# Optimization experiments

Measured on AMD Instinct MI355X. Metric: run time of the kernel, lower is better.

## Reference

```python
import jax, jax.numpy as jnp
import numpy as np

D_MODEL, D_K, D_V = 512, 64, 64
B, S = 8, 4096


def setup_inputs() -> dict:
    key = jax.random.key(0)
    ks = jax.random.split(key, 10)
    scale = 1.0 / np.sqrt(D_MODEL)
    return {
        "q": jax.random.normal(ks[0], (B, S, D_MODEL), dtype=jnp.float32),
        "k": jax.random.normal(ks[1], (B, S, D_MODEL), dtype=jnp.float32),
        "v": jax.random.normal(ks[2], (B, S, D_MODEL), dtype=jnp.float32),
        "mask": jax.random.randint(ks[3], (B, S), 0, 2, dtype=jnp.int32),
        "Wq": jax.random.uniform(ks[4], (D_MODEL, D_K), jnp.float32, -scale, scale),
        "bq": jax.random.uniform(ks[5], (D_K,), jnp.float32, -scale, scale),
        "Wk": jax.random.uniform(ks[6], (D_MODEL, D_K), jnp.float32, -scale, scale),
        "bk": jax.random.uniform(ks[7], (D_K,), jnp.float32, -scale, scale),
        "Wv": jax.random.uniform(ks[8], (D_MODEL, D_V), jnp.float32, -scale, scale),
        "bv": jax.random.uniform(ks[9], (D_V,), jnp.float32, -scale, scale),
    }


def reference(q, k, v, mask, Wq, bq, Wk, bk, Wv, bv):
    # single-head QKV projections
    qh = jnp.einsum("bsd,dk->bsk", q, Wq) + bq  # [B,S,d_k]
    kh = jnp.einsum("bsd,dk->bsk", k, Wk) + bk  # [B,S,d_k]
    vh = jnp.einsum("bsd,dv->bsv", v, Wv) + bv  # [B,S,d_v]
    scores = jnp.einsum("bqk,bsk->bqs", qh, kh) / jnp.sqrt(jnp.float32(D_K))
    # key-padding mask: mask [B,S] -> [B,1,S], masked positions -> -1e10
    scores = jnp.where(mask[:, None, :] == 0, jnp.float32(-1e10), scores)
    attn = jax.nn.softmax(scores, axis=-1)
    return jnp.einsum("bqs,bsv->bqv", attn, vh)
```

## Files before the change

kernel.cpp:

```cpp
#include <hip/hip_runtime.h>

typedef __attribute__((ext_vector_type(8))) short bf16x8;
typedef __attribute__((ext_vector_type(4))) float f32x4;
typedef __attribute__((ext_vector_type(4))) unsigned short u16x4;

__device__ __forceinline__ short f2bf(float f) {
  unsigned int u = __builtin_bit_cast(unsigned int, f);
  u += 0x7fffu + ((u >> 16) & 1u);
  return (short)(u >> 16);
}

__global__ void prep_w(const float* __restrict__ Wq, const float* __restrict__ Wk,
                       const float* __restrict__ Wv, unsigned short* __restrict__ wt) {
  int idx = blockIdx.x * 256 + threadIdx.x;
  int m = idx >> 15;
  int rem = idx & 32767;
  int n = rem >> 9;
  int k = rem & 511;
  const float* W = (m == 0) ? Wq : ((m == 1) ? Wk : Wv);
  wt[idx] = (unsigned short)f2bf(W[k * 64 + n]);
}

__global__ __launch_bounds__(256) void proj_kernel(
    const float* __restrict__ qx, const float* __restrict__ kx, const float* __restrict__ vx,
    const unsigned short* __restrict__ wt, const int* __restrict__ mask,
    const float* __restrict__ bqp, const float* __restrict__ bkp, const float* __restrict__ bvp,
    unsigned short* __restrict__ qo, unsigned short* __restrict__ ko,
    unsigned short* __restrict__ vo) {
  __shared__ unsigned short lds[64 * 256];
  const int mode = blockIdx.y;
  const float* x = (mode == 0) ? qx : ((mode == 1) ? kx : vx);
  const float* bias = (mode == 0) ? bqp : ((mode == 1) ? bkp : bvp);
  const unsigned short* wtm = wt + mode * (64 * 512);
  const float osc = (mode == 0) ? 0.18033688011112042f : 1.0f;

  const int tid = threadIdx.x;
  const int w = tid >> 6, lane = tid & 63;
  const int g = lane >> 4, ln = lane & 15;
  const int rowbase = blockIdx.x * 128;

  const f32x4 fz = {0.f, 0.f, 0.f, 0.f};
  f32x4 acc[2][4];
#pragma unroll
  for (int mi = 0; mi < 2; ++mi)
#pragma unroll
    for (int nf = 0; nf < 4; ++nf) acc[mi][nf] = fz;

  for (int half = 0; half < 2; ++half) {
    __syncthreads();
#pragma unroll
    for (int i = 0; i < 8; ++i) {
      int c = tid + i * 256;
      int n = c >> 5, kc = c & 31;
      bf16x8 d = *reinterpret_cast<const bf16x8*>(wtm + n * 512 + half * 256 + kc * 8);
      int bo = (n * 512 + kc * 16) ^ ((n & 7) << 4);
      *reinterpret_cast<bf16x8*>(reinterpret_cast<char*>(lds) + bo) = d;
    }
    __syncthreads();
#pragma unroll
    for (int ks = 0; ks < 8; ++ks) {
      bf16x8 afrag[2];
#pragma unroll
      for (int mi = 0; mi < 2; ++mi) {
        int row = rowbase + w * 32 + mi * 16 + ln;
        const float4* ap = reinterpret_cast<const float4*>(
            x + (size_t)row * 512 + half * 256 + ks * 32 + g * 8);
        float4 a0 = ap[0], a1 = ap[1];
        bf16x8 af;
        af[0] = f2bf(a0.x); af[1] = f2bf(a0.y); af[2] = f2bf(a0.z); af[3] = f2bf(a0.w);
        af[4] = f2bf(a1.x); af[5] = f2bf(a1.y); af[6] = f2bf(a1.z); af[7] = f2bf(a1.w);
        afrag[mi] = af;
      }
#pragma unroll
      for (int nf = 0; nf < 4; ++nf) {
        int n = nf * 16 + ln;
        int bo = (n * 512 + ks * 64 + g * 16) ^ ((n & 7) << 4);
        bf16x8 bfrag = *reinterpret_cast<const bf16x8*>(reinterpret_cast<const char*>(lds) + bo);
        acc[0][nf] = __builtin_amdgcn_mfma_f32_16x16x32_bf16(afrag[0], bfrag, acc[0][nf], 0, 0, 0);
        acc[1][nf] = __builtin_amdgcn_mfma_f32_16x16x32_bf16(afrag[1], bfrag, acc[1][nf], 0, 0, 0);
      }
    }
  }

  float bc[4];
#pragma unroll
  for (int nf = 0; nf < 4; ++nf) bc[nf] = bias[nf * 16 + ln];

  if (mode < 2) {
    unsigned short* o = (mode == 0) ? qo : ko;
#pragma unroll
    for (int mi = 0; mi < 2; ++mi)
#pragma unroll
      for (int nf = 0; nf < 4; ++nf)
#pragma unroll
        for (int r = 0; r < 4; ++r) {
          int row = rowbase + w * 32 + mi * 16 + g * 4 + r;
          o[(size_t)row * 64 + nf * 16 + ln] = (unsigned short)f2bf((acc[mi][nf][r] + bc[nf]) * osc);
        }
  } else {
    __syncthreads();
#pragma unroll
    for (int mi = 0; mi < 2; ++mi)
#pragma unroll
      for (int nf = 0; nf < 4; ++nf)
#pragma unroll
        for (int r = 0; r < 4; ++r) {
          int srow = w * 32 + mi * 16 + g * 4 + r;
          lds[srow * 64 + nf * 16 + ln] = (unsigned short)f2bf(acc[mi][nf][r] + bc[nf]);
        }
    __syncthreads();
    int b = rowbase >> 12, s0 = rowbase & 4095;
    int dv = tid & 63, sc = tid >> 6;
#pragma unroll
    for (int i = 0; i < 4; ++i) {
      int sbase = s0 + sc * 32 + i * 8;
      const int* mrow = mask + b * 4096 + sbase;
      bf16x8 pack;
#pragma unroll
      for (int j = 0; j < 8; ++j) {
        short vv = (short)lds[(sc * 32 + i * 8 + j) * 64 + dv];
        pack[j] = mrow[j] ? vv : (short)0;
      }
      *reinterpret_cast<bf16x8*>(vo + (size_t)(b * 64 + dv) * 4096 + sbase) = pack;
    }
  }
}

#define KVBLK 128
#define NT 16

__global__ __launch_bounds__(256, 2) void attn_kernel(
    const unsigned short* __restrict__ qh, const unsigned short* __restrict__ kh,
    const unsigned short* __restrict__ vt, const int* __restrict__ mask,
    float* __restrict__ out0, float* __restrict__ out1,
    float* __restrict__ l0p, float* __restrict__ l1p) {
  __shared__ unsigned short kt[2][KVBLK * 64];
  __shared__ unsigned short vv[2][80 * 128];

  const int b = blockIdx.y;
  const int z = blockIdx.z;
  const int kv0 = z * (NT * KVBLK);
  float* __restrict__ optr = z ? out1 : out0;
  float* __restrict__ lptr = z ? l1p : l0p;
  const int qbase = blockIdx.x * 128;
  const int tid = threadIdx.x;
  const int w = tid >> 6, lane = tid & 63;
  const int g = lane >> 4, ln = lane & 15;

  for (int i = tid; i < 15 * 128; i += 256) {
    vv[0][65 * 128 + i] = 0;
    vv[1][65 * 128 + i] = 0;
  }

  bf16x8 qa[2][2];
#pragma unroll
  for (int qf = 0; qf < 2; ++qf) {
    int row = qbase + w * 32 + qf * 16 + ln;
    const unsigned short* qp = qh + (size_t)(b * 4096 + row) * 64;
    qa[qf][0] = *reinterpret_cast<const bf16x8*>(qp + g * 8);
    qa[qf][1] = *reinterpret_cast<const bf16x8*>(qp + 32 + g * 8);
  }

  const f32x4 fz = {0.f, 0.f, 0.f, 0.f};
  f32x4 accO[2][5];
#pragma unroll
  for (int qf = 0; qf < 2; ++qf)
#pragma unroll
    for (int nf = 0; nf < 5; ++nf) accO[qf][nf] = fz;

  const unsigned short* khb = kh + (size_t)b * 4096 * 64;
  const unsigned short* vtb = vt + (size_t)b * 64 * 4096;

  bf16x8 kreg[4], vreg[4];
  int mreg = 0;
  auto issue = [&](int ti) {
    int kvbase = kv0 + ti * KVBLK;
#pragma unroll
    for (int i = 0; i < 4; ++i) {
      int c = tid + i * 256;
      vreg[i] = *reinterpret_cast<const bf16x8*>(vtb + (size_t)(c >> 4) * 4096 + kvbase + (c & 15) * 8);
      kreg[i] = *reinterpret_cast<const bf16x8*>(khb + (size_t)(kvbase + (c >> 3)) * 64 + (c & 7) * 8);
    }
    if (tid < KVBLK) mreg = mask[b * 4096 + kvbase + tid];
  };
  auto commit = [&](int bs) {
#pragma unroll
    for (int i = 0; i < 4; ++i) {
      int c = tid + i * 256;
      int kbo = ((c >> 3) * 128 + (c & 7) * 16) ^ (((c >> 3) & 7) << 4);
      *reinterpret_cast<bf16x8*>(reinterpret_cast<char*>(kt[bs]) + kbo) = kreg[i];
      int dv = c >> 4;
      int P0 = (c & 15) * 8;
      int c2 = P0 >> 5, h = (P0 >> 4) & 1, gg = (P0 >> 2) & 3;
      int x1 = 32 * c2 + 8 * gg + 4 * h;
      int swz = (dv & 7) << 4;
      union { bf16x8 v; u16x4 h4[2]; } sp; sp.v = vreg[i];
      *reinterpret_cast<u16x4*>(reinterpret_cast<char*>(vv[bs]) + ((dv * 256 + 2 * x1) ^ swz)) = sp.h4[0];
      *reinterpret_cast<u16x4*>(reinterpret_cast<char*>(vv[bs]) + ((dv * 256 + 2 * x1 + 16) ^ swz)) = sp.h4[1];
    }
    if (tid < KVBLK) {
      int p = tid;
      int x = 32 * (p >> 5) + 8 * ((p >> 2) & 3) + 4 * ((p >> 4) & 1) + (p & 3);
      vv[bs][64 * 128 + x] = mreg ? (unsigned short)0x3F80 : (unsigned short)0;
    }
  };

  issue(0);
  commit(0);
  __syncthreads();
  int cur = 0;

  for (int ti = 0; ti < NT; ++ti) {
    if (ti + 1 < NT) issue(ti + 1);

    f32x4 s0[8], s1[8];
#pragma unroll
    for (int nf = 0; nf < 8; ++nf) { s0[nf] = fz; s1[nf] = fz; }
    __builtin_amdgcn_s_setprio(1);
#pragma unroll
    for (int c2 = 0; c2 < 2; ++c2)
#pragma unroll
      for (int nf = 0; nf < 8; ++nf) {
        int kvr = nf * 16 + ln;
        int bo = (kvr * 128 + c2 * 64 + g * 16) ^ ((kvr & 7) << 4);
        bf16x8 kf = *reinterpret_cast<const bf16x8*>(reinterpret_cast<const char*>(kt[cur]) + bo);
        s0[nf] = __builtin_amdgcn_mfma_f32_16x16x32_bf16(kf, qa[0][c2], s0[nf], 0, 0, 0);
        s1[nf] = __builtin_amdgcn_mfma_f32_16x16x32_bf16(kf, qa[1][c2], s1[nf], 0, 0, 0);
      }
    __builtin_amdgcn_s_setprio(0);

    unsigned int pw[2][4][4];
#pragma unroll
    for (int c2 = 0; c2 < 4; ++c2)
#pragma unroll
      for (int hh = 0; hh < 2; ++hh) {
        {
          float p0 = __builtin_exp2f(s0[2 * c2 + hh][0]);
          float p1 = __builtin_exp2f(s0[2 * c2 + hh][1]);
          float p2 = __builtin_exp2f(s0[2 * c2 + hh][2]);
          float p3 = __builtin_exp2f(s0[2 * c2 + hh][3]);
          unsigned int w0, w1;
          asm("v_cvt_pk_bf16_f32 %0, %1, %2" : "=v"(w0) : "v"(p0), "v"(p1));
          asm("v_cvt_pk_bf16_f32 %0, %1, %2" : "=v"(w1) : "v"(p2), "v"(p3));
          pw[0][c2][2 * hh] = w0;
          pw[0][c2][2 * hh + 1] = w1;
        }
        {
          float p0 = __builtin_exp2f(s1[2 * c2 + hh][0]);
          float p1 = __builtin_exp2f(s1[2 * c2 + hh][1]);
          float p2 = __builtin_exp2f(s1[2 * c2 + hh][2]);
          float p3 = __builtin_exp2f(s1[2 * c2 + hh][3]);
          unsigned int w0, w1;
          asm("v_cvt_pk_bf16_f32 %0, %1, %2" : "=v"(w0) : "v"(p0), "v"(p1));
          asm("v_cvt_pk_bf16_f32 %0, %1, %2" : "=v"(w1) : "v"(p2), "v"(p3));
          pw[1][c2][2 * hh] = w0;
          pw[1][c2][2 * hh + 1] = w1;
        }
      }

    __builtin_amdgcn_s_setprio(1);
#pragma unroll
    for (int c2 = 0; c2 < 4; ++c2) {
      union { unsigned int u[4]; bf16x8 v; } pa0, pa1;
#pragma unroll
      for (int t = 0; t < 4; ++t) { pa0.u[t] = pw[0][c2][t]; pa1.u[t] = pw[1][c2][t]; }
#pragma unroll
      for (int nf = 0; nf < 5; ++nf) {
        int dvr = nf * 16 + ln;
        int bo = (dvr * 256 + c2 * 64 + g * 16) ^ ((dvr & 7) << 4);
        bf16x8 vb = *reinterpret_cast<const bf16x8*>(reinterpret_cast<const char*>(vv[cur]) + bo);
        accO[0][nf] = __builtin_amdgcn_mfma_f32_16x16x32_bf16(pa0.v, vb, accO[0][nf], 0, 0, 0);
        accO[1][nf] = __builtin_amdgcn_mfma_f32_16x16x32_bf16(pa1.v, vb, accO[1][nf], 0, 0, 0);
      }
    }
    __builtin_amdgcn_s_setprio(0);

    if (ti + 1 < NT) commit(cur ^ 1);
    __syncthreads();
    cur ^= 1;
  }

#pragma unroll
  for (int qf = 0; qf < 2; ++qf)
#pragma unroll
    for (int r = 0; r < 4; ++r) {
      int grow = b * 4096 + qbase + w * 32 + qf * 16 + g * 4 + r;
#pragma unroll
      for (int nf = 0; nf < 4; ++nf)
        optr[(size_t)grow * 64 + nf * 16 + ln] = accO[qf][nf][r];
      if (ln == 0) lptr[grow] = accO[qf][4][r];
    }
}

__global__ __launch_bounds__(256) void combine_kernel(
    float* __restrict__ out, const float* __restrict__ po1,
    const float* __restrict__ l0p, const float* __restrict__ l1p) {
  int idx = blockIdx.x * 256 + threadIdx.x;
  int row = idx >> 4;
  float rl = 1.0f / (l0p[row] + l1p[row]);
  float4 a = reinterpret_cast<float4*>(out)[idx];
  float4 c = reinterpret_cast<const float4*>(po1)[idx];
  a.x = (a.x + c.x) * rl;
  a.y = (a.y + c.y) * rl;
  a.z = (a.z + c.z) * rl;
  a.w = (a.w + c.w) * rl;
  reinterpret_cast<float4*>(out)[idx] = a;
}

extern "C" void kernel_launch(void* const* d_in, const int* in_sizes, int n_in,
                              void* d_out, int out_size, void* d_ws, size_t ws_size,
                              hipStream_t stream) {
  const float* q = (const float*)d_in[0];
  const float* k = (const float*)d_in[1];
  const float* v = (const float*)d_in[2];
  const int* mask = (const int*)d_in[3];
  const float* Wq = (const float*)d_in[4];
  const float* bq = (const float*)d_in[5];
  const float* Wk = (const float*)d_in[6];
  const float* bk = (const float*)d_in[7];
  const float* Wv = (const float*)d_in[8];
  const float* bv = (const float*)d_in[9];

  char* wsb = (char*)d_ws;
  unsigned short* qh = (unsigned short*)(wsb);
  unsigned short* kh = (unsigned short*)(wsb + (4u << 20));
  unsigned short* vt = (unsigned short*)(wsb + (8u << 20));
  unsigned short* wt = (unsigned short*)(wsb + (12u << 20));
  float* po1 = (float*)(wsb + (12u << 20) + 196608);
  float* l0p = (float*)(wsb + (12u << 20) + 196608 + (8u << 20));
  float* l1p = l0p + 32768;

  prep_w<<<384, 256, 0, stream>>>(Wq, Wk, Wv, wt);
  proj_kernel<<<dim3(256, 3), 256, 0, stream>>>(q, k, v, wt, mask, bq, bk, bv, qh, kh, vt);
  attn_kernel<<<dim3(32, 8, 2), 256, 0, stream>>>(qh, kh, vt, mask,
                                                  (float*)d_out, po1, l0p, l1p);
  combine_kernel<<<2048, 256, 0, stream>>>((float*)d_out, po1, l0p, l1p);
}
```

Baseline: 111.8 us.

## Halve projection tile rows, prefetch activations, and raise occupancy

The projection kernel now handles 64 rows per block instead of 128, launching twice as many blocks, and sets launch bounds to target 5 blocks per CU. The activation loads are software-pipelined: each iteration issues the next k-slice's float4 loads before converting and multiplying the current one. The second weight half is staged mid-loop. This is meant to hide global-memory latency on the memory-bound fp32 activation stream, at the cost of staging the weights twice as often across blocks.

New measurement: 111.2 us. About the same (-0.6%).

```diff
diff --git a/kernel.cpp b/kernel.cpp
--- a/kernel.cpp
+++ b/kernel.cpp
@@ -21,7 +21,7 @@
   wt[idx] = (unsigned short)f2bf(W[k * 64 + n]);
 }
 
-__global__ __launch_bounds__(256) void proj_kernel(
+__global__ __launch_bounds__(256, 5) void proj_kernel(
     const float* __restrict__ qx, const float* __restrict__ kx, const float* __restrict__ vx,
     const unsigned short* __restrict__ wt, const int* __restrict__ mask,
     const float* __restrict__ bqp, const float* __restrict__ bkp, const float* __restrict__ bvp,
@@ -37,17 +37,16 @@
   const int tid = threadIdx.x;
   const int w = tid >> 6, lane = tid & 63;
   const int g = lane >> 4, ln = lane & 15;
-  const int rowbase = blockIdx.x * 128;
+  const int rowbase = blockIdx.x * 64;
 
   const f32x4 fz = {0.f, 0.f, 0.f, 0.f};
-  f32x4 acc[2][4];
-#pragma unroll
-  for (int mi = 0; mi < 2; ++mi)
-#pragma unroll
-    for (int nf = 0; nf < 4; ++nf) acc[mi][nf] = fz;
-
-  for (int half = 0; half < 2; ++half) {
-    __syncthreads();
+  f32x4 acc[4];
+#pragma unroll
+  for (int nf = 0; nf < 4; ++nf) acc[nf] = fz;
+
+  const float* xrow = x + (size_t)(rowbase + w * 16 + ln) * 512 + g * 8;
+
+  auto stageW = [&](int half) {
 #pragma unroll
     for (int i = 0; i < 8; ++i) {
       int c = tid + i * 256;
@@ -56,30 +55,39 @@
       int bo = (n * 512 + kc * 16) ^ ((n & 7) << 4);
       *reinterpret_cast<bf16x8*>(reinterpret_cast<char*>(lds) + bo) = d;
     }
-    __syncthreads();
-#pragma unroll
-    for (int ks = 0; ks < 8; ++ks) {
-      bf16x8 afrag[2];
-#pragma unroll
-      for (int mi = 0; mi < 2; ++mi) {
-        int row = rowbase + w * 32 + mi * 16 + ln;
-        const float4* ap = reinterpret_cast<const float4*>(
-            x + (size_t)row * 512 + half * 256 + ks * 32 + g * 8);
-        float4 a0 = ap[0], a1 = ap[1];
-        bf16x8 af;
-        af[0] = f2bf(a0.x); af[1] = f2bf(a0.y); af[2] = f2bf(a0.z); af[3] = f2bf(a0.w);
-        af[4] = f2bf(a1.x); af[5] = f2bf(a1.y); af[6] = f2bf(a1.z); af[7] = f2bf(a1.w);
-        afrag[mi] = af;
-      }
-#pragma unroll
-      for (int nf = 0; nf < 4; ++nf) {
-        int n = nf * 16 + ln;
-        int bo = (n * 512 + ks * 64 + g * 16) ^ ((n & 7) << 4);
-        bf16x8 bfrag = *reinterpret_cast<const bf16x8*>(reinterpret_cast<const char*>(lds) + bo);
-        acc[0][nf] = __builtin_amdgcn_mfma_f32_16x16x32_bf16(afrag[0], bfrag, acc[0][nf], 0, 0, 0);
-        acc[1][nf] = __builtin_amdgcn_mfma_f32_16x16x32_bf16(afrag[1], bfrag, acc[1][nf], 0, 0, 0);
-      }
-    }
+  };
+
+  stageW(0);
+  float4 xa = reinterpret_cast<const float4*>(xrow)[0];
+  float4 xb = reinterpret_cast<const float4*>(xrow)[1];
+  __syncthreads();
+
+#pragma unroll
+  for (int t = 0; t < 16; ++t) {
+    float4 na, nb;
+    if (t < 15) {
+      const float4* np = reinterpret_cast<const float4*>(xrow + (t + 1) * 32);
+      na = np[0];
+      nb = np[1];
+    }
+    if (t == 8) {
+      __syncthreads();
+      stageW(1);
+      __syncthreads();
+    }
+    bf16x8 af;
+    af[0] = f2bf(xa.x); af[1] = f2bf(xa.y); af[2] = f2bf(xa.z); af[3] = f2bf(xa.w);
+    af[4] = f2bf(xb.x); af[5] = f2bf(xb.y); af[6] = f2bf(xb.z); af[7] = f2bf(xb.w);
+    int ks = t & 7;
+#pragma unroll
+    for (int nf = 0; nf < 4; ++nf) {
+      int n = nf * 16 + ln;
+      int bo = (n * 512 + ks * 64 + g * 16) ^ ((n & 7) << 4);
+      bf16x8 bfrag = *reinterpret_cast<const bf16x8*>(reinterpret_cast<const char*>(lds) + bo);
+      acc[nf] = __builtin_amdgcn_mfma_f32_16x16x32_bf16(af, bfrag, acc[nf], 0, 0, 0);
+    }
+    xa = na;
+    xb = nb;
   }
 
   float bc[4];
@@ -89,37 +97,33 @@
   if (mode < 2) {
     unsigned short* o = (mode == 0) ? qo : ko;
 #pragma unroll
-    for (int mi = 0; mi < 2; ++mi)
-#pragma unroll
-      for (int nf = 0; nf < 4; ++nf)
-#pragma unroll
-        for (int r = 0; r < 4; ++r) {
-          int row = rowbase + w * 32 + mi * 16 + g * 4 + r;
-          o[(size_t)row * 64 + nf * 16 + ln] = (unsigned short)f2bf((acc[mi][nf][r] + bc[nf]) * osc);
-        }
+    for (int nf = 0; nf < 4; ++nf)
+#pragma unroll
+      for (int r = 0; r < 4; ++r) {
+        int row = rowbase + w * 16 + g * 4 + r;
+        o[(size_t)row * 64 + nf * 16 + ln] = (unsigned short)f2bf((acc[nf][r] + bc[nf]) * osc);
+      }
   } else {
     __syncthreads();
 #pragma unroll
-    for (int mi = 0; mi < 2; ++mi)
-#pragma unroll
-      for (int nf = 0; nf < 4; ++nf)
-#pragma unroll
-        for (int r = 0; r < 4; ++r) {
-          int srow = w * 32 + mi * 16 + g * 4 + r;
-          lds[srow * 64 + nf * 16 + ln] = (unsigned short)f2bf(acc[mi][nf][r] + bc[nf]);
-        }
+    for (int nf = 0; nf < 4; ++nf)
+#pragma unroll
+      for (int r = 0; r < 4; ++r) {
+        int srow = w * 16 + g * 4 + r;
+        lds[srow * 64 + nf * 16 + ln] = (unsigned short)f2bf(acc[nf][r] + bc[nf]);
+      }
     __syncthreads();
     int b = rowbase >> 12, s0 = rowbase & 4095;
     int dv = tid & 63, sc = tid >> 6;
 #pragma unroll
-    for (int i = 0; i < 4; ++i) {
-      int sbase = s0 + sc * 32 + i * 8;
+    for (int i = 0; i < 2; ++i) {
+      int sbase = s0 + sc * 16 + i * 8;
       const int* mrow = mask + b * 4096 + sbase;
       bf16x8 pack;
 #pragma unroll
       for (int j = 0; j < 8; ++j) {
-        short vv = (short)lds[(sc * 32 + i * 8 + j) * 64 + dv];
-        pack[j] = mrow[j] ? vv : (short)0;
+        short vvv = (short)lds[(sc * 16 + i * 8 + j) * 64 + dv];
+        pack[j] = mrow[j] ? vvv : (short)0;
       }
       *reinterpret_cast<bf16x8*>(vo + (size_t)(b * 64 + dv) * 4096 + sbase) = pack;
     }
@@ -331,7 +335,7 @@
   float* l1p = l0p + 32768;
 
   prep_w<<<384, 256, 0, stream>>>(Wq, Wk, Wv, wt);
-  proj_kernel<<<dim3(256, 3), 256, 0, stream>>>(q, k, v, wt, mask, bq, bk, bv, qh, kh, vt);
+  proj_kernel<<<dim3(512, 3), 256, 0, stream>>>(q, k, v, wt, mask, bq, bk, bv, qh, kh, vt);
   attn_kernel<<<dim3(32, 8, 2), 256, 0, stream>>>(qh, kh, vt, mask,
                                                   (float*)d_out, po1, l0p, l1p);
   combine_kernel<<<2048, 256, 0, stream>>>((float*)d_out, po1, l0p, l1p);
```
